# Optimization experiments

Hardware: AMD Instinct MI355X
Metric: run time of the kernel (lower is better)

Reference implementation:

```python
import jax, jax.numpy as jnp
import numpy as np

NEG_SLOPE = 0.01  # torch LeakyReLU default

def leaky_relu(x):
    return jnp.where(x >= 0, x, NEG_SLOPE * x)

def setup_inputs() -> dict:
    key = jax.random.key(0)
    ks = jax.random.split(key, 12)
    D = 128
    N_U, N_I, E = 100000, 50000, 1000000
    s = 1.0 / np.sqrt(D)
    return {
        "h_user": jax.random.normal(ks[0], (N_U, D), jnp.float32),
        "h_item": jax.random.normal(ks[1], (N_I, D), jnp.float32),
        "src_idx": jax.random.randint(ks[2], (E,), 0, N_U, jnp.int64) if jax.config.jax_enable_x64 else jax.random.randint(ks[2], (E,), 0, N_U, jnp.int32),
        "dst_idx": jax.random.randint(ks[3], (E,), 0, N_I, jnp.int32),
        "W_left": jax.random.normal(ks[4], (D, D), jnp.float32) * s,
        "b_left": jax.random.normal(ks[5], (D,), jnp.float32) * s,
        "W_right": jax.random.normal(ks[6], (D, D), jnp.float32) * s,
        "b_right": jax.random.normal(ks[7], (D,), jnp.float32) * s,
        "W1": jax.random.normal(ks[8], (D, D), jnp.float32) * s,
        "b1": jax.random.normal(ks[9], (D,), jnp.float32) * s,
        "W2": jax.random.normal(ks[10], (D, 1), jnp.float32) * s,
        "b2": jax.random.normal(ks[11], (1,), jnp.float32) * s,
    }

def reference(h_user, h_item, src_idx, dst_idx,
              W_left, b_left, W_right, b_right, W1, b1, W2, b2):
    # node linear transforms (dropout is identity in eval mode)
    u_f = h_user @ W_left + b_left      # [N_u, D]
    i_f = h_item @ W_right + b_right    # [N_i, D]
    # edge gather + add (dgl fn.u_add_v)
    score = u_f[src_idx] + i_f[dst_idx]  # [E, D]
    # pred MLP: LeakyReLU -> Linear(D,D) -> LeakyReLU -> Linear(D,1) -> LeakyReLU
    x = leaky_relu(score)
    x = leaky_relu(x @ W1 + b1)
    x = leaky_relu(x @ W2 + b2)         # [E, 1]
    return x
```

## Files before the change

### kernel.cpp

```cpp
#include <hip/hip_runtime.h>

typedef __attribute__((ext_vector_type(8))) short bf16x8;
typedef __attribute__((ext_vector_type(4))) float f32x4;
typedef __attribute__((ext_vector_type(2))) float f32x2;

__device__ __forceinline__ float leaky(float v) { return fmaxf(v, 0.01f * v); }

__device__ __forceinline__ unsigned short f2bf(float a) {
    unsigned int u = __float_as_uint(a);
    return (unsigned short)((u + 0x7FFFu + ((u >> 16) & 1u)) >> 16);
}

__device__ __forceinline__ unsigned int cvtpk(float a, float b) {
#if __has_builtin(__builtin_amdgcn_cvt_pk_bf16_f32)
    typedef __attribute__((ext_vector_type(2))) __bf16 bf2_t;
    bf2_t v = __builtin_amdgcn_cvt_pk_bf16_f32(a, b);
    return __builtin_bit_cast(unsigned int, v);
#else
    unsigned int ua = __float_as_uint(a);
    ua = (ua + 0x7FFFu + ((ua >> 16) & 1u)) >> 16;
    unsigned int ub = __float_as_uint(b);
    ub = (ub + 0x7FFFu + ((ub >> 16) & 1u)) >> 16;
    return ua | (ub << 16);
#endif
}

__device__ __forceinline__ f32x2 unpk2(unsigned int d) {
    f32x2 r;
    r.x = __uint_as_float(d << 16);
    r.y = __uint_as_float(d & 0xFFFF0000u);
    return r;
}

__device__ __forceinline__ unsigned int mix1(unsigned int u, unsigned int i) {
    f32x2 v = unpk2(u) + unpk2(i);
    v = __builtin_elementwise_max(v, v * 0.01f);
    return cvtpk(v.x, v.y);
}

__global__ __launch_bounds__(128) void prep(const float* __restrict__ WL,
                                            const float* __restrict__ WR,
                                            const float* __restrict__ W1,
                                            unsigned short* __restrict__ WLf,
                                            unsigned short* __restrict__ WRf,
                                            unsigned short* __restrict__ Wf) {
    int g = blockIdx.x;
    int f = (g & 127) * 128 + threadIdx.x;
    int j = f & 7, lane = (f >> 3) & 63, nt = (f >> 9) & 7, kb = f >> 12;
    int n = nt * 16 + (lane & 15);
    int kf = kb * 32 + (lane >> 4) * 8 + j;
    if (g < 128) {
        WLf[f] = f2bf(WL[kf * 128 + n]);
    } else if (g < 256) {
        WRf[f] = f2bf(WR[kf * 128 + n]);
    } else {
        int k = (kf & 7) * 16 + (kf >> 3);
        Wf[f] = f2bf(W1[k * 128 + n]);
    }
}

#define PITCH 136

__global__ __launch_bounds__(512, 6) void node_mfma2(const float* __restrict__ h_user,
                                                     const float* __restrict__ h_item,
                                                     const unsigned short* __restrict__ WLf,
                                                     const unsigned short* __restrict__ WRf,
                                                     const float* __restrict__ b_left,
                                                     const float* __restrict__ b_right,
                                                     unsigned short* __restrict__ u_f,
                                                     unsigned short* __restrict__ i_f,
                                                     int N_U, int N_I, int BU) {
    bool isU = (int)blockIdx.x < BU;
    const float* h = isU ? h_user : h_item;
    const unsigned short* Wfr = isU ? WLf : WRf;
    const float* b = isU ? b_left : b_right;
    unsigned short* out = isU ? u_f : i_f;
    int N = isU ? N_U : N_I;
    int r0 = (isU ? blockIdx.x : blockIdx.x - BU) * 128;

    __shared__ __attribute__((aligned(16))) unsigned short xt[128 * PITCH];
    int t = threadIdx.x;
    int s = t & 31;
    int el0 = t >> 5;

    f32x4 g[8];
#pragma unroll
    for (int pass = 0; pass < 8; ++pass) {
        int row = min(r0 + pass * 16 + el0, N - 1);
        g[pass] = *(const f32x4*)(h + (size_t)row * 128 + s * 4);
    }
#pragma unroll
    for (int pass = 0; pass < 8; ++pass) {
        int el = pass * 16 + el0;
        unsigned int* rp = (unsigned int*)(xt + el * PITCH + s * 4);
        rp[0] = cvtpk(g[pass].x, g[pass].y);
        rp[1] = cvtpk(g[pass].z, g[pass].w);
    }
    __syncthreads();

    int wave = t >> 6;
    int lane = t & 63;
    int col = lane & 15;
    int quad = lane >> 4;
    int wp = wave >> 1;
    int ch = wave & 1;
    int m0 = wp * 32;

    f32x4 acc[2][4];
#pragma unroll
    for (int mt = 0; mt < 2; ++mt)
#pragma unroll
        for (int i = 0; i < 4; ++i) acc[mt][i] = (f32x4){0.f, 0.f, 0.f, 0.f};

#pragma unroll
    for (int kb = 0; kb < 4; ++kb) {
        bf16x8 afr[2];
#pragma unroll
        for (int mt = 0; mt < 2; ++mt)
            afr[mt] = *(const bf16x8*)(xt + (m0 + mt * 16 + col) * PITCH + kb * 32 + quad * 8);
#pragma unroll
        for (int i = 0; i < 4; ++i) {
            int nt = ch * 4 + i;
            bf16x8 bfr = *(const bf16x8*)(Wfr + ((kb * 8 + nt) * 64 + lane) * 8);
            acc[0][i] = __builtin_amdgcn_mfma_f32_16x16x32_bf16(afr[0], bfr, acc[0][i], 0, 0, 0);
            acc[1][i] = __builtin_amdgcn_mfma_f32_16x16x32_bf16(afr[1], bfr, acc[1][i], 0, 0, 0);
        }
    }

    float bb[4];
#pragma unroll
    for (int i = 0; i < 4; ++i) bb[i] = b[(ch * 4 + i) * 16 + col];

    __syncthreads();

#pragma unroll
    for (int mt = 0; mt < 2; ++mt)
#pragma unroll
        for (int rr = 0; rr < 4; ++rr) {
            int row = m0 + mt * 16 + quad * 4 + rr;
            uint2 v;
            v.x = cvtpk(acc[mt][0][rr] + bb[0], acc[mt][1][rr] + bb[1]);
            v.y = cvtpk(acc[mt][2][rr] + bb[2], acc[mt][3][rr] + bb[3]);
            *(uint2*)(xt + (size_t)row * PITCH + col * 8 + ch * 4) = v;
        }
    __syncthreads();

    {
        int row = t >> 2;
        int seg = t & 3;
        if (r0 + row < N) {
            const uint4* lp = (const uint4*)(xt + (size_t)row * PITCH + seg * 32);
            uint4* gp = (uint4*)(out + (size_t)(r0 + row) * 128 + seg * 32);
            uint4 a0 = lp[0], a1 = lp[1], a2 = lp[2], a3 = lp[3];
            gp[0] = a0; gp[1] = a1; gp[2] = a2; gp[3] = a3;
        }
    }
}

#define TE 128

__global__ __launch_bounds__(512, 6) void edge_kernel(
    const unsigned short* __restrict__ u_f, const unsigned short* __restrict__ i_f,
    const int* __restrict__ src, const int* __restrict__ dst,
    const unsigned short* __restrict__ Wf,
    const float* __restrict__ b1, const float* __restrict__ W2,
    const float* __restrict__ b2, float* __restrict__ out, int E, int bofs) {
    __shared__ unsigned short xt[TE * PITCH];
    __shared__ float zb[4][2][32];
    int t = threadIdx.x;
    int e0 = (blockIdx.x + bofs) * TE;

    int s = t & 15;
    int el0 = t >> 4;

    int wave = t >> 6;
    int lane = t & 63;
    int col = lane & 15;
    int quad = lane >> 4;
    int wp = wave >> 1;
    int ch = wave & 1;
    int m0 = wp * 32;

    float bb[4], ww[4];
#pragma unroll
    for (int i = 0; i < 4; ++i) {
        int n = (ch * 4 + i) * 16 + col;
        bb[i] = b1[n];
        ww[i] = W2[n];
    }
    float b2v = b2[0];

    int su[4], sd[4];
#pragma unroll
    for (int pass = 0; pass < 4; ++pass) {
        int ec = min(e0 + pass * 32 + el0, E - 1);
        su[pass] = src[ec];
        sd[pass] = dst[ec];
    }
    {
        uint4 ug[4], ig[4];
#pragma unroll
        for (int pass = 0; pass < 4; ++pass) {
            ug[pass] = *(const uint4*)(u_f + (size_t)su[pass] * 128 + s * 8);
            ig[pass] = *(const uint4*)(i_f + (size_t)sd[pass] * 128 + s * 8);
        }
#pragma unroll
        for (int pass = 0; pass < 4; ++pass) {
            uint4 a;
            a.x = mix1(ug[pass].x, ig[pass].x);
            a.y = mix1(ug[pass].y, ig[pass].y);
            a.z = mix1(ug[pass].z, ig[pass].z);
            a.w = mix1(ug[pass].w, ig[pass].w);
            *(uint4*)(xt + (pass * 32 + el0) * PITCH + s * 8) = a;
        }
    }
    __syncthreads();

    f32x4 acc[2][4];
#pragma unroll
    for (int mt = 0; mt < 2; ++mt)
#pragma unroll
        for (int i = 0; i < 4; ++i)
            acc[mt][i] = (f32x4){bb[i], bb[i], bb[i], bb[i]};

#pragma unroll
    for (int kb = 0; kb < 4; ++kb) {
        bf16x8 afr[2];
#pragma unroll
        for (int mt = 0; mt < 2; ++mt)
            afr[mt] = *(const bf16x8*)(xt + (m0 + mt * 16 + col) * PITCH + kb * 32 + quad * 8);
#pragma unroll
        for (int i = 0; i < 4; ++i) {
            int nt = ch * 4 + i;
            bf16x8 bfr = *(const bf16x8*)(Wf + ((kb * 8 + nt) * 64 + lane) * 8);
            acc[0][i] = __builtin_amdgcn_mfma_f32_16x16x32_bf16(afr[0], bfr, acc[0][i], 0, 0, 0);
            acc[1][i] = __builtin_amdgcn_mfma_f32_16x16x32_bf16(afr[1], bfr, acc[1][i], 0, 0, 0);
        }
    }

    f32x4 pz[2];
#pragma unroll
    for (int mt = 0; mt < 2; ++mt) pz[mt] = (f32x4){0.f, 0.f, 0.f, 0.f};

#pragma unroll
    for (int i = 0; i < 4; ++i) {
#pragma unroll
        for (int mt = 0; mt < 2; ++mt) {
            f32x4 y = acc[mt][i];
            y = __builtin_elementwise_max(y, y * 0.01f);
            pz[mt] += y * ww[i];
        }
    }
#pragma unroll
    for (int off = 1; off < 16; off <<= 1)
#pragma unroll
        for (int mt = 0; mt < 2; ++mt)
#pragma unroll
            for (int rr = 0; rr < 4; ++rr) pz[mt][rr] += __shfl_xor(pz[mt][rr], off, 64);

    if (col == 0) {
#pragma unroll
        for (int mt = 0; mt < 2; ++mt)
#pragma unroll
            for (int rr = 0; rr < 4; ++rr)
                zb[wp][ch][mt * 16 + quad * 4 + rr] = pz[mt][rr];
    }
    __syncthreads();

    if (t < 128) {
        int g = t >> 5;
        int idx = t & 31;
        float z = zb[g][0][idx] + zb[g][1][idx] + b2v;
        int e = e0 + g * 32 + idx;
        if (e < E) out[e] = leaky(z);
    }
}

extern "C" void kernel_launch(void* const* d_in, const int* in_sizes, int n_in,
                              void* d_out, int out_size, void* d_ws, size_t ws_size,
                              hipStream_t stream) {
    const float* h_user  = (const float*)d_in[0];
    const float* h_item  = (const float*)d_in[1];
    const int*   src_idx = (const int*)d_in[2];
    const int*   dst_idx = (const int*)d_in[3];
    const float* W_left  = (const float*)d_in[4];
    const float* b_left  = (const float*)d_in[5];
    const float* W_right = (const float*)d_in[6];
    const float* b_right = (const float*)d_in[7];
    const float* W1      = (const float*)d_in[8];
    const float* b1      = (const float*)d_in[9];
    const float* W2      = (const float*)d_in[10];
    const float* b2      = (const float*)d_in[11];
    float* out = (float*)d_out;

    int N_U = in_sizes[0] / 128;
    int N_I = in_sizes[1] / 128;
    int E   = in_sizes[2];

    unsigned short* Wf  = (unsigned short*)d_ws;
    unsigned short* WLf = Wf + 16384;
    unsigned short* WRf = WLf + 16384;
    unsigned short* u_f = (unsigned short*)((char*)d_ws + 131072);
    unsigned short* i_f = u_f + (size_t)N_U * 128;

    prep<<<384, 128, 0, stream>>>(W_left, W_right, W1, WLf, WRf, Wf);

    int BU = (N_U + 127) / 128;
    int BI = (N_I + 127) / 128;
    node_mfma2<<<BU + BI, 512, 0, stream>>>(h_user, h_item, WLf, WRf, b_left, b_right,
                                            u_f, i_f, N_U, N_I, BU);

    int NBLK = (E + TE - 1) / TE;
    int C = (NBLK + 1) / 2;
    for (int part = 0; part < 2; ++part) {
        int bofs = part * C;
        int nb = NBLK - bofs;
        if (nb <= 0) break;
        if (nb > C) nb = C;
        edge_kernel<<<nb, 512, 0, stream>>>(u_f, i_f, src_idx, dst_idx,
                                            Wf, b1, W2, b2, out, E, bofs);
    }
}
```

Measured before the change: 237.5 us.

## Bucket edges by source-node range to improve gather locality in edge kernel

Adds a histogram, scan and atomic scatter pass that groups edges into 196 buckets by source index (512 users per bucket). The edge kernel then processes each bucket with 48 persistent blocks, interleaved so concurrently running blocks share a bucket. The aim is to make u_f row gathers hit cache instead of random DRAM reads. In exchange it adds three extra kernels, atomic-heavy scattering of 3M ints and an indirect output write through a permutation array, and the bucket grid assumes fixed sizes (196 buckets, 9600 blocks).

```diff
diff --git a/kernel.cpp b/kernel.cpp
--- a/kernel.cpp
+++ b/kernel.cpp
@@ -3,6 +3,9 @@
 typedef __attribute__((ext_vector_type(8))) short bf16x8;
 typedef __attribute__((ext_vector_type(4))) float f32x4;
 typedef __attribute__((ext_vector_type(2))) float f32x2;
+
+#define NBUK 196
+#define BSTR 32
 
 __device__ __forceinline__ float leaky(float v) { return fmaxf(v, 0.01f * v); }
 
@@ -43,9 +46,15 @@
                                             const float* __restrict__ W1,
                                             unsigned short* __restrict__ WLf,
                                             unsigned short* __restrict__ WRf,
-                                            unsigned short* __restrict__ Wf) {
+                                            unsigned short* __restrict__ Wf,
+                                            int* __restrict__ bins) {
     int g = blockIdx.x;
-    int f = (g & 127) * 128 + threadIdx.x;
+    int t = threadIdx.x;
+    if (g == 0) {
+        if (t < NBUK) bins[t * BSTR] = 0;
+        if (t + 128 < NBUK) bins[(t + 128) * BSTR] = 0;
+    }
+    int f = (g & 127) * 128 + t;
     int j = f & 7, lane = (f >> 3) & 63, nt = (f >> 9) & 7, kb = f >> 12;
     int n = nt * 16 + (lane & 15);
     int kf = kb * 32 + (lane >> 4) * 8 + j;
@@ -56,6 +65,54 @@
     } else {
         int k = (kf & 7) * 16 + (kf >> 3);
         Wf[f] = f2bf(W1[k * 128 + n]);
+    }
+}
+
+__global__ __launch_bounds__(256) void hist(const int* __restrict__ src,
+                                            int* __restrict__ bins, int E) {
+    __shared__ int lb[NBUK];
+    int t = threadIdx.x;
+    if (t < NBUK) lb[t] = 0;
+    __syncthreads();
+    for (int e = blockIdx.x * 256 + t; e < E; e += gridDim.x * 256)
+        atomicAdd(&lb[src[e] >> 9], 1);
+    __syncthreads();
+    if (t < NBUK && lb[t]) atomicAdd(&bins[t * BSTR], lb[t]);
+}
+
+__global__ __launch_bounds__(256) void scan196(const int* __restrict__ bins,
+                                               int* __restrict__ base,
+                                               int* __restrict__ cur) {
+    __shared__ int sc[256];
+    int t = threadIdx.x;
+    int v = (t < NBUK) ? bins[t * BSTR] : 0;
+    sc[t] = v;
+    __syncthreads();
+    for (int off = 1; off < 256; off <<= 1) {
+        int x = (t >= off) ? sc[t - off] : 0;
+        __syncthreads();
+        sc[t] += x;
+        __syncthreads();
+    }
+    if (t < NBUK) {
+        int ex = sc[t] - v;
+        base[t] = ex;
+        cur[t * BSTR] = ex;
+    }
+}
+
+__global__ __launch_bounds__(256) void scatter(const int* __restrict__ src,
+                                               const int* __restrict__ dst,
+                                               int* __restrict__ cur,
+                                               int* __restrict__ sb,
+                                               int* __restrict__ db,
+                                               int* __restrict__ pe, int E) {
+    for (int e = blockIdx.x * 256 + threadIdx.x; e < E; e += gridDim.x * 256) {
+        int s_ = src[e], d_ = dst[e];
+        int slot = atomicAdd(&cur[(s_ >> 9) * BSTR], 1);
+        sb[slot] = s_;
+        db[slot] = d_;
+        pe[slot] = e;
     }
 }
 
@@ -161,15 +218,26 @@
 
 __global__ __launch_bounds__(512, 6) void edge_kernel(
     const unsigned short* __restrict__ u_f, const unsigned short* __restrict__ i_f,
-    const int* __restrict__ src, const int* __restrict__ dst,
+    const int* __restrict__ sb, const int* __restrict__ db,
+    const int* __restrict__ pe,
+    const int* __restrict__ bins, const int* __restrict__ base,
     const unsigned short* __restrict__ Wf,
     const float* __restrict__ b1, const float* __restrict__ W2,
-    const float* __restrict__ b2, float* __restrict__ out, int E, int bofs) {
+    const float* __restrict__ b2, float* __restrict__ out, int E) {
+    int p = blockIdx.x;
+    int x = p & 7;
+    int q = p >> 3;
+    int j = q / 48;
+    int t0 = q % 48;
+    int b = x + (j << 3);
+    if (b >= NBUK) return;
+    int cnt = bins[b * BSTR];
+    if (cnt == 0) return;
+    int bs = base[b];
+
     __shared__ unsigned short xt[TE * PITCH];
     __shared__ float zb[4][2][32];
     int t = threadIdx.x;
-    int e0 = (blockIdx.x + bofs) * TE;
-
     int s = t & 15;
     int el0 = t >> 4;
 
@@ -190,89 +258,95 @@
     }
     float b2v = b2[0];
 
-    int su[4], sd[4];
-#pragma unroll
-    for (int pass = 0; pass < 4; ++pass) {
-        int ec = min(e0 + pass * 32 + el0, E - 1);
-        su[pass] = src[ec];
-        sd[pass] = dst[ec];
-    }
-    {
-        uint4 ug[4], ig[4];
+    for (int tt = t0; tt * TE < cnt; tt += 48) {
+        int s0 = tt * TE;
+
+        int su[4], sd[4];
 #pragma unroll
         for (int pass = 0; pass < 4; ++pass) {
-            ug[pass] = *(const uint4*)(u_f + (size_t)su[pass] * 128 + s * 8);
-            ig[pass] = *(const uint4*)(i_f + (size_t)sd[pass] * 128 + s * 8);
-        }
-#pragma unroll
-        for (int pass = 0; pass < 4; ++pass) {
-            uint4 a;
-            a.x = mix1(ug[pass].x, ig[pass].x);
-            a.y = mix1(ug[pass].y, ig[pass].y);
-            a.z = mix1(ug[pass].z, ig[pass].z);
-            a.w = mix1(ug[pass].w, ig[pass].w);
-            *(uint4*)(xt + (pass * 32 + el0) * PITCH + s * 8) = a;
-        }
-    }
-    __syncthreads();
-
-    f32x4 acc[2][4];
-#pragma unroll
-    for (int mt = 0; mt < 2; ++mt)
-#pragma unroll
-        for (int i = 0; i < 4; ++i)
-            acc[mt][i] = (f32x4){bb[i], bb[i], bb[i], bb[i]};
-
-#pragma unroll
-    for (int kb = 0; kb < 4; ++kb) {
-        bf16x8 afr[2];
+            int sc = bs + min(s0 + pass * 32 + el0, cnt - 1);
+            su[pass] = sb[sc];
+            sd[pass] = db[sc];
+        }
+        {
+            uint4 ug[4], ig[4];
+#pragma unroll
+            for (int pass = 0; pass < 4; ++pass) {
+                ug[pass] = *(const uint4*)(u_f + (size_t)su[pass] * 128 + s * 8);
+                ig[pass] = *(const uint4*)(i_f + (size_t)sd[pass] * 128 + s * 8);
+            }
+#pragma unroll
+            for (int pass = 0; pass < 4; ++pass) {
+                uint4 a;
+                a.x = mix1(ug[pass].x, ig[pass].x);
+                a.y = mix1(ug[pass].y, ig[pass].y);
+                a.z = mix1(ug[pass].z, ig[pass].z);
+                a.w = mix1(ug[pass].w, ig[pass].w);
+                *(uint4*)(xt + (pass * 32 + el0) * PITCH + s * 8) = a;
+            }
+        }
+        __syncthreads();
+
+        f32x4 acc[2][4];
 #pragma unroll
         for (int mt = 0; mt < 2; ++mt)
-            afr[mt] = *(const bf16x8*)(xt + (m0 + mt * 16 + col) * PITCH + kb * 32 + quad * 8);
+#pragma unroll
+            for (int i = 0; i < 4; ++i)
+                acc[mt][i] = (f32x4){bb[i], bb[i], bb[i], bb[i]};
+
+#pragma unroll
+        for (int kb = 0; kb < 4; ++kb) {
+            bf16x8 afr[2];
+#pragma unroll
+            for (int mt = 0; mt < 2; ++mt)
+                afr[mt] = *(const bf16x8*)(xt + (m0 + mt * 16 + col) * PITCH + kb * 32 + quad * 8);
+#pragma unroll
+            for (int i = 0; i < 4; ++i) {
+                int nt = ch * 4 + i;
+                bf16x8 bfr = *(const bf16x8*)(Wf + ((kb * 8 + nt) * 64 + lane) * 8);
+                acc[0][i] = __builtin_amdgcn_mfma_f32_16x16x32_bf16(afr[0], bfr, acc[0][i], 0, 0, 0);
+                acc[1][i] = __builtin_amdgcn_mfma_f32_16x16x32_bf16(afr[1], bfr, acc[1][i], 0, 0, 0);
+            }
+        }
+
+        f32x4 pz[2];
+#pragma unroll
+        for (int mt = 0; mt < 2; ++mt) pz[mt] = (f32x4){0.f, 0.f, 0.f, 0.f};
+
 #pragma unroll
         for (int i = 0; i < 4; ++i) {
-            int nt = ch * 4 + i;
-            bf16x8 bfr = *(const bf16x8*)(Wf + ((kb * 8 + nt) * 64 + lane) * 8);
-            acc[0][i] = __builtin_amdgcn_mfma_f32_16x16x32_bf16(afr[0], bfr, acc[0][i], 0, 0, 0);
-            acc[1][i] = __builtin_amdgcn_mfma_f32_16x16x32_bf16(afr[1], bfr, acc[1][i], 0, 0, 0);
-        }
-    }
-
-    f32x4 pz[2];
-#pragma unroll
-    for (int mt = 0; mt < 2; ++mt) pz[mt] = (f32x4){0.f, 0.f, 0.f, 0.f};
-
-#pragma unroll
-    for (int i = 0; i < 4; ++i) {
-#pragma unroll
-        for (int mt = 0; mt < 2; ++mt) {
-            f32x4 y = acc[mt][i];
-            y = __builtin_elementwise_max(y, y * 0.01f);
-            pz[mt] += y * ww[i];
-        }
-    }
-#pragma unroll
-    for (int off = 1; off < 16; off <<= 1)
-#pragma unroll
-        for (int mt = 0; mt < 2; ++mt)
-#pragma unroll
-            for (int rr = 0; rr < 4; ++rr) pz[mt][rr] += __shfl_xor(pz[mt][rr], off, 64);
-
-    if (col == 0) {
-#pragma unroll
-        for (int mt = 0; mt < 2; ++mt)
-#pragma unroll
-            for (int rr = 0; rr < 4; ++rr)
-                zb[wp][ch][mt * 16 + quad * 4 + rr] = pz[mt][rr];
-    }
-    __syncthreads();
-
-    if (t < 128) {
-        int g = t >> 5;
-        int idx = t & 31;
-        float z = zb[g][0][idx] + zb[g][1][idx] + b2v;
-        int e = e0 + g * 32 + idx;
-        if (e < E) out[e] = leaky(z);
+#pragma unroll
+            for (int mt = 0; mt < 2; ++mt) {
+                f32x4 y = acc[mt][i];
+                y = __builtin_elementwise_max(y, y * 0.01f);
+                pz[mt] += y * ww[i];
+            }
+        }
+#pragma unroll
+        for (int off = 1; off < 16; off <<= 1)
+#pragma unroll
+            for (int mt = 0; mt < 2; ++mt)
+#pragma unroll
+                for (int rr = 0; rr < 4; ++rr) pz[mt][rr] += __shfl_xor(pz[mt][rr], off, 64);
+
+        if (col == 0) {
+#pragma unroll
+            for (int mt = 0; mt < 2; ++mt)
+#pragma unroll
+                for (int rr = 0; rr < 4; ++rr)
+                    zb[wp][ch][mt * 16 + quad * 4 + rr] = pz[mt][rr];
+        }
+        __syncthreads();
+
+        if (t < 128) {
+            int sl = s0 + t;
+            if (sl < cnt) {
+                int g2 = t >> 5;
+                int idx = t & 31;
+                float z = zb[g2][0][idx] + zb[g2][1][idx] + b2v;
+                out[pe[bs + sl]] = leaky(z);
+            }
+        }
     }
 }
 
@@ -302,22 +376,25 @@
     unsigned short* WRf = WLf + 16384;
     unsigned short* u_f = (unsigned short*)((char*)d_ws + 131072);
     unsigned short* i_f = u_f + (size_t)N_U * 128;
-
-    prep<<<384, 128, 0, stream>>>(W_left, W_right, W1, WLf, WRf, Wf);
+    size_t mo = (131072 + (size_t)(N_U + N_I) * 256 + 4095) & ~(size_t)4095;
+    int* bins = (int*)((char*)d_ws + mo);
+    int* base = (int*)((char*)d_ws + mo + 32768);
+    int* cur  = (int*)((char*)d_ws + mo + 36864);
+    int* sb   = (int*)((char*)d_ws + mo + 69632);
+    int* db   = sb + E;
+    int* pe   = db + E;
+
+    prep<<<384, 128, 0, stream>>>(W_left, W_right, W1, WLf, WRf, Wf, bins);
+
+    hist<<<256, 256, 0, stream>>>(src_idx, bins, E);
+    scan196<<<1, 256, 0, stream>>>(bins, base, cur);
+    scatter<<<1024, 256, 0, stream>>>(src_idx, dst_idx, cur, sb, db, pe, E);
 
     int BU = (N_U + 127) / 128;
     int BI = (N_I + 127) / 128;
     node_mfma2<<<BU + BI, 512, 0, stream>>>(h_user, h_item, WLf, WRf, b_left, b_right,
                                             u_f, i_f, N_U, N_I, BU);
 
-    int NBLK = (E + TE - 1) / TE;
-    int C = (NBLK + 1) / 2;
-    for (int part = 0; part < 2; ++part) {
-        int bofs = part * C;
-        int nb = NBLK - bofs;
-        if (nb <= 0) break;
-        if (nb > C) nb = C;
-        edge_kernel<<<nb, 512, 0, stream>>>(u_f, i_f, src_idx, dst_idx,
-                                            Wf, b1, W2, b2, out, E, bofs);
-    }
-}
+    edge_kernel<<<9600, 512, 0, stream>>>(u_f, i_f, sb, db, pe, bins, base,
+                                          Wf, b1, W2, b2, out, E);
+}
```

Result: slower. 678.2 us (+185.6%).
